# Performance work log

Hardware: AMD Instinct MI355X
Metric: run time of the kernel (lower is better)

## Reference

```python
import jax, jax.numpy as jnp
import numpy as np

NEG = -1e9  # acts as -inf in the DP while staying finite for grads


def nw_value(theta, A):
    """Soft Needleman-Wunsch terminal value with softmax (logsumexp) operator.
    theta: [N, M] match scores; A: scalar gap score.
    Recurrence: V[i,j] = theta[i-1,j-1] + logsumexp(V[i-1,j]+A, V[i-1,j-1], V[i,j-1]+A)
    with V[0,0]=0 and V[i,0]=V[0,j]=-inf.
    """
    N, M = theta.shape
    init_row = jnp.full((M + 1,), NEG, theta.dtype).at[0].set(0.0)

    def row_step(prev_row, theta_row):
        def col_step(v_left, inp):
            th, v_diag, v_up = inp
            v = th + jnp.logaddexp(jnp.logaddexp(v_up + A, v_diag), v_left + A)
            return v, v
        _, row = jax.lax.scan(
            col_step, jnp.asarray(NEG, theta.dtype),
            (theta_row, prev_row[:-1], prev_row[1:]))
        new_row = jnp.concatenate([jnp.full((1,), NEG, theta.dtype), row])
        return new_row, None

    last_row, _ = jax.lax.scan(row_step, init_row, theta)
    return last_row[M]


def nw_decode(theta, A):
    # Soft alignment matrix = dV/dtheta (expected alignment under softmax operator),
    # matching NeedlemanWunschDecoder.decode.
    return jax.grad(nw_value)(theta, A)


def setup_inputs() -> dict:
    key = jax.random.key(0)
    ks = jax.random.split(key, 7)
    B, N, M = 8, 1024, 1024
    n_alpha, n_input, n_embed = 22, 512, 512
    x = jax.random.randint(ks[0], (B, N), 0, n_alpha)
    y = jax.random.randint(ks[1], (B, M), 0, n_alpha)
    emb = jax.random.normal(ks[2], (n_alpha, n_input), jnp.float32)
    W = jax.random.normal(ks[3], (n_input, n_embed), jnp.float32) / np.sqrt(n_input)
    b = jax.random.normal(ks[4], (n_embed,), jnp.float32) * 0.01
    Wg = jax.random.normal(ks[5], (2 * n_embed, 1), jnp.float32) / np.sqrt(2 * n_embed)
    bg = jax.random.normal(ks[6], (1,), jnp.float32) * 0.01
    return {"x": x, "y": y, "emb": emb, "W": W, "b": b, "Wg": Wg, "bg": bg}


def reference(x, y, emb, W, b, Wg, bg):
    zx = emb[x] @ W + b                       # [B, N, d] embedding (EmbedLinear)
    zy = emb[y] @ W + b                       # [B, M, d]
    theta = jnp.einsum('bid,bjd->bij', zx, zy)   # [B, N, M] pairwise match scores
    merged = jnp.concatenate([zx.mean(axis=1), zy.mean(axis=1)], axis=1)  # [B, 2d]
    A = merged @ Wg + bg                      # [B, 1] gap score
    aln = jax.vmap(nw_decode)(theta, A[:, 0])    # [B, N, M]
    return jnp.swapaxes(aln, 1, 2)               # [B, M, N] (decode(...).T per batch)
```

## Files before the change

kernel.cpp:

```cpp
#include <hip/hip_runtime.h>
#include <cstdint>
#include <cstddef>

#define NEGV -1.0e9f
#define WAVES 16

__device__ __forceinline__ float lse_f(float a, float b) {
    float d = a - b;
    float m = fmaxf(a, b);
    return m + log1pf(expf(-fabsf(d)));
}
__device__ __forceinline__ float cellfwd(float th, float vu, float vdg, float vl, float A) {
    float inner = lse_f(vu + A, vdg);
    float outer = lse_f(inner, vl + A);
    return th + outer;
}

__device__ __forceinline__ void diag_geo(int d, int& st, int& L, int& tlo) {
    if (d < 64)        { st = (d * (d + 1)) >> 1;       L = d + 1;      tlo = 0; }
    else if (d < 1024) { st = 2080 + ((d - 64) << 6);   L = 64;         tlo = 0; }
    else               { int u = d - 1024;
                         st = 63520 + (u << 6) - ((u * (u + 1)) >> 1);
                         L = 63 - u;                    tlo = u + 1; }
}

__global__ void k_embed(const float* __restrict__ emb, const float* __restrict__ W,
                        const float* __restrict__ b, double* __restrict__ T) {
    int idx = blockIdx.x * blockDim.x + threadIdx.x;
    if (idx >= 22 * 512) return;
    int a = idx >> 9, d = idx & 511;
    double acc = (double)b[d];
    const float* er = emb + a * 512;
    for (int k = 0; k < 512; ++k) acc += (double)er[k] * (double)W[k * 512 + d];
    T[idx] = acc;
}

__global__ void k_gau(const double* __restrict__ T, const int* __restrict__ x,
                      const int* __restrict__ y, const float* __restrict__ Wg,
                      const float* __restrict__ bg,
                      double* __restrict__ G, double* __restrict__ Aout) {
    __shared__ double u1s[22], u2s[22];
    int t = threadIdx.x;
    if (t < 484) {
        int a = t / 22, c = t % 22;
        const double* ra = T + a * 512;
        const double* rc = T + c * 512;
        double acc = 0.0;
        for (int d = 0; d < 512; ++d) acc += ra[d] * rc[d];
        G[t] = acc;
    }
    if (t < 22) {
        double acc = 0.0;
        const double* ra = T + t * 512;
        for (int d = 0; d < 512; ++d) acc += ra[d] * (double)Wg[d];
        u1s[t] = acc;
    } else if (t >= 64 && t < 86) {
        int a = t - 64;
        double acc = 0.0;
        const double* ra = T + a * 512;
        for (int d = 0; d < 512; ++d) acc += ra[d] * (double)Wg[512 + d];
        u2s[a] = acc;
    }
    __syncthreads();
    int w = t >> 6, lane = t & 63;
    const int* xb = x + w * 1024;
    const int* yb = y + w * 1024;
    double s = 0.0;
    for (int i = lane; i < 1024; i += 64) s += u1s[xb[i]] + u2s[yb[i]];
    for (int off = 32; off > 0; off >>= 1) s += __shfl_down(s, off);
    if (lane == 0) Aout[w] = s * (1.0 / 1024.0) + (double)bg[0];
}

__global__ void k_vinit(float* __restrict__ Vbuf) {
    int b = blockIdx.x, t = threadIdx.x;
    float* Vb = Vbuf + (size_t)b * (1025 * 1025);
    Vb[t] = (t == 0) ? 0.0f : NEGV;
    if (t == 0) Vb[1024] = NEGV;
    Vb[(size_t)(t + 1) * 1025] = NEGV;
}

__global__ __launch_bounds__(1024) void k_fwdb(const int* __restrict__ x,
                                               const int* __restrict__ y,
                                               const double* __restrict__ G,
                                               const double* __restrict__ Aarr,
                                               float* __restrict__ Vbuf) {
    __shared__ float Gs[484];
    __shared__ int ys_s[1024];
    __shared__ float topbuf[WAVES][1024];
    __shared__ int prog[WAVES];

    const int b = blockIdx.x;
    const int tid = threadIdx.x;
    const int w = tid >> 6;
    const int t = tid & 63;
    float* Vb = Vbuf + (size_t)b * (1025 * 1025);

    if (tid < 484) Gs[tid] = (float)G[tid];
    ys_s[tid] = y[(b << 10) + tid];
    if (tid < WAVES) prog[tid] = 0;
    const int xs = x[(b << 10) + tid];
    __syncthreads();

    const float A = (float)Aarr[b];
    const float* Grow = Gs + xs * 22;
    float* vst = Vb + (size_t)(tid + 1) * 1025 + 1;

    float vp = NEGV;
    float vdgc = (tid == 0) ? 0.0f : NEGV;

    for (int s = 0; s < 1024 + 63; ++s) {
        if (w > 0 && s < 1024 && (s & 15) == 0) {
            const int target = (s + 16 < 1024) ? s + 16 : 1024;
            while (__hip_atomic_load(&prog[w], __ATOMIC_ACQUIRE,
                                     __HIP_MEMORY_SCOPE_WORKGROUP) < target)
                __builtin_amdgcn_s_sleep(1);
        }
        const float vu_lds = (w > 0) ? topbuf[w][(s < 1024) ? s : 1023] : NEGV;
        const float ush = __shfl_up(vp, 1);
        const int j = s - t + 1;
        if (j >= 1 && j <= 1024) {
            float vu  = (t == 0) ? vu_lds : ush;
            float v = cellfwd(Grow[ys_s[j - 1]], vu, vdgc, vp, A);
            vst[j - 1] = v;
            if (w < WAVES - 1 && t == 63) {
                topbuf[w + 1][j - 1] = v;
                if ((j & 15) == 0)
                    __hip_atomic_store(&prog[w + 1], j, __ATOMIC_RELEASE,
                                       __HIP_MEMORY_SCOPE_WORKGROUP);
            }
            vp = v; vdgc = vu;
        }
    }
}

__global__ __launch_bounds__(256) void k_wb(const double* __restrict__ Aarr,
                                            const float* __restrict__ Vbuf,
                                            float* __restrict__ bw) {
    int idx = blockIdx.x * 256 + threadIdx.x;
    int b = idx >> 20;
    int cell = idx & 1048575;
    int i = (cell >> 10) + 1;
    int j = (cell & 1023) + 1;
    const float* Vb = Vbuf + (size_t)b * (1025 * 1025);
    float vu  = Vb[(size_t)(i - 1) * 1025 + j];
    float vdg = Vb[(size_t)(i - 1) * 1025 + (j - 1)];
    float vl  = Vb[(size_t)i * 1025 + (j - 1)];
    float A = (float)Aarr[b];
    float t1 = vu + A;
    float t2 = vl + A;
    float di = t1 - vdg;
    float inner = (di > 0.f) ? (t1  + log1pf(expf(-di)))
                             : (vdg + log1pf(expf(di)));
    float dw = inner - t2;
    float outer = (dw > 0.f) ? (inner + log1pf(expf(-dw)))
                             : (t2    + log1pf(expf(dw)));
    float go1 = expf(inner - outer);
    float wlW = expf(t2 - outer);
    float wuW = go1 * expf(t1 - inner);
    float wdW = go1 * expf(vdg - inner);
    float* bbp = bw + (size_t)b * 3145728;

    if (i >= 2) {
        int rb = (i - 2) >> 4, q = (i - 2) & 15, cj = j - 1;
        int st, L, tlo; diag_geo(rb + cj, st, L, tlo);
        int f = 3 * q;
        bbp[(size_t)st * 48 + (size_t)(f >> 2) * 4 * L + ((rb - tlo) << 2) + (f & 3)] = wuW;
    }
    if (i >= 2 && j >= 2) {
        int rb = (i - 2) >> 4, q = (i - 2) & 15, cj = j - 2;
        int st, L, tlo; diag_geo(rb + cj, st, L, tlo);
        int f = 3 * q + 1;
        bbp[(size_t)st * 48 + (size_t)(f >> 2) * 4 * L + ((rb - tlo) << 2) + (f & 3)] = wdW;
    }
    if (j >= 2) {
        int rb = (i - 1) >> 4, q = (i - 1) & 15, cj = j - 2;
        int st, L, tlo; diag_geo(rb + cj, st, L, tlo);
        int f = 3 * q + 2;
        bbp[(size_t)st * 48 + (size_t)(f >> 2) * 4 * L + ((rb - tlo) << 2) + (f & 3)] = wlW;
    }
}

__global__ __launch_bounds__(64) void k_bwd16(const float* __restrict__ bw,
                                              float* __restrict__ out) {
    const int t = threadIdx.x;
    const int b = blockIdx.x;
    const float* bb = bw + (size_t)b * 3145728;
    float* ob = out + ((size_t)b << 20);
    const int r0 = t << 4;

    float e[16];
    float4 cwv[12], pfv[12];
    #pragma unroll
    for (int q = 0; q < 16; ++q) e[q] = 0.f;

    {
        int st, L, tlo; diag_geo(t + 1023, st, L, tlo);
        const float* base = bb + (size_t)st * 48;
        #pragma unroll
        for (int k = 0; k < 12; ++k)
            cwv[k] = *(const float4*)(base + (size_t)k * 4 * L);
    }

    float sdb = 0.f;
    for (int s = 0; s < 1087; ++s) {
        float dn = __shfl_down(e[0], 1);
        const int d = 1086 - s;
        const int cj = d - t;
        if (cj >= 0 && cj < 1024) {
            {
                int st, L, tlo; diag_geo(d - 1, st, L, tlo);
                const int p = t - tlo;
                const float* base = bb + (size_t)st * 48 + ((size_t)p << 2);
                #pragma unroll
                for (int k = 0; k < 12; ++k)
                    pfv[k] = *(const float4*)(base + (size_t)k * 4 * L);
            }
            const float* F = (const float*)cwv;

            float old_b = e[15];
            float eu = (t == 63) ? 0.f : dn;
            float ed = (t == 63) ? 0.f : sdb;
            float v = eu * F[45] + ed * F[46] + old_b * F[47];
            if (t == 63 && cj == 1023) v = 1.0f;
            e[15] = v;
            float new_b = v;
            #pragma unroll
            for (int q = 14; q >= 0; --q) {
                float oq = e[q];
                v = new_b * F[3 * q] + old_b * F[3 * q + 1] + oq * F[3 * q + 2];
                e[q] = v;
                new_b = v; old_b = oq;
            }
            #pragma unroll
            for (int k = 0; k < 4; ++k)
                *(float4*)&ob[(size_t)cj * 1024 + r0 + 4 * k] =
                    make_float4(e[4*k], e[4*k+1], e[4*k+2], e[4*k+3]);
            #pragma unroll
            for (int k = 0; k < 12; ++k) cwv[k] = pfv[k];
        }
        sdb = dn;
    }
}

template <bool FAITHFUL>
__global__ __launch_bounds__(1024) void k_dp(const int* __restrict__ x,
                                             const int* __restrict__ y,
                                             const double* __restrict__ G,
                                             const double* __restrict__ Aarr,
                                             float2* __restrict__ wbuf,
                                             float* __restrict__ wdbuf,
                                             float* __restrict__ out) {
    __shared__ float Gs[484];
    __shared__ int xs[1024], ys[1024];
    __shared__ float D[3][1025];
    __shared__ float E[3][1026];

    const int b = blockIdx.x;
    const int t = threadIdx.x;
    const int i = t + 1;

    if (t < 484) Gs[t] = (float)G[t];
    xs[t] = x[(b << 10) + t];
    ys[t] = y[(b << 10) + t];
    D[0][t + 1] = NEGV;
    D[1][t + 1] = NEGV;
    E[0][t] = 0.f; E[1][t] = 0.f; E[2][t] = 0.f;
    if (t == 0) {
        D[0][0] = 0.0f;
        D[1][0] = NEGV;
        E[0][1024] = 0.f; E[0][1025] = 0.f;
        E[1][1024] = 0.f; E[1][1025] = 0.f;
        E[2][1024] = 0.f; E[2][1025] = 0.f;
    }
    __syncthreads();

    const float A = (float)Aarr[b];
    const float* Grow = Gs + xs[t] * 22;
    float2* wb = wbuf + ((size_t)b << 20);
    float*  wdb = wdbuf + ((size_t)b << 20);

    for (int k = 2; k <= 2048; ++k) {
        const int cur = k % 3, p1 = (k + 2) % 3, p2 = (k + 1) % 3;
        const int j = k - i;
        if (j >= 1 && j <= 1024) {
            float vu  = D[p1][i - 1];
            float vdg = D[p2][i - 1];
            float vl  = D[p1][i];
            float t1 = vu + A;
            float t2 = vl + A;
            float di = t1 - vdg;
            float inner = (di > 0.f) ? (t1  + log1pf(expf(-di)))
                                     : (vdg + log1pf(expf(di)));
            float dw = inner - t2;
            float outer = (dw > 0.f) ? (inner + log1pf(expf(-dw)))
                                     : (t2    + log1pf(expf(dw)));
            D[cur][i] = Grow[ys[j - 1]] + outer;
            float go1 = expf(inner - outer);
            float wlW = expf(t2 - outer);
            float wuW = go1 * expf(t1 - inner);
            size_t ci = ((size_t)t << 10) + (j - 1);
            wb[ci] = make_float2(wuW, wlW);
            if (FAITHFUL) wdb[ci] = go1 * expf(vdg - inner);
        }
        if (t == 0) D[cur][0] = NEGV;
        if (i == k && k <= 1024) D[cur][k] = NEGV;
        __syncthreads();
    }

    __syncthreads();

    float* ob = out + ((size_t)b << 20);

    for (int k = 2048; k >= 2; --k) {
        const int cur = k % 3, n1 = (k + 1) % 3, n2 = (k + 2) % 3;
        const int j = k - i;
        if (j >= 1 && j <= 1024) {
            float e;
            if (k == 2048) {
                e = 1.0f;
            } else {
                float Eu = E[n1][i + 1];
                float Ed = E[n2][i + 1];
                float El = E[n1][i];
                int iw = (i < 1024) ? i : 1023;
                int jw = (j < 1024) ? j : 1023;
                float2 w_up = wb[((size_t)iw << 10) + (j - 1)];
                float2 w_lf = wb[((size_t)(i - 1) << 10) + jw];
                float w_dd;
                if (FAITHFUL) {
                    w_dd = wdb[((size_t)iw << 10) + jw];
                } else {
                    float2 w_dg = wb[((size_t)iw << 10) + jw];
                    w_dd = 1.0f - w_dg.x - w_dg.y;
                }
                e = Eu * w_up.x + Ed * w_dd + El * w_lf.y;
            }
            E[cur][i] = e;
            ob[((size_t)(j - 1) << 10) + (i - 1)] = e;
        } else {
            E[cur][i] = 0.f;
        }
        __syncthreads();
    }
}

extern "C" void kernel_launch(void* const* d_in, const int* in_sizes, int n_in,
                              void* d_out, int out_size, void* d_ws, size_t ws_size,
                              hipStream_t stream) {
    const int*   x   = (const int*)d_in[0];
    const int*   y   = (const int*)d_in[1];
    const float* emb = (const float*)d_in[2];
    const float* W   = (const float*)d_in[3];
    const float* b   = (const float*)d_in[4];
    const float* Wg  = (const float*)d_in[5];
    const float* bg  = (const float*)d_in[6];
    float* out = (float*)d_out;

    char* ws = (char*)d_ws;
    double* T    = (double*)(ws + 0);
    double* G    = (double*)(ws + 90112);
    double* Aarr = (double*)(ws + 94336);
    float*  bund = (float*)(ws + 131072);
    float2* wbuf = (float2*)(ws + 131072);
    float*  wdbuf = (float*)(ws + 131072 + ((size_t)64 << 20));
    float*  Vbuf = (float*)(ws + 131072 + ((size_t)96 << 20));

    k_embed<<<44, 256, 0, stream>>>(emb, W, b, T);
    k_gau<<<1, 512, 0, stream>>>(T, x, y, Wg, bg, G, Aarr);

    const size_t need_old = 131072 + ((size_t)96 << 20);
    const size_t need_new = need_old + (size_t)8 * 1025 * 1025 * 4;

    if (ws_size >= need_new) {
        k_vinit<<<8, 1024, 0, stream>>>(Vbuf);
        k_fwdb<<<8, 1024, 0, stream>>>(x, y, G, Aarr, Vbuf);
        k_wb<<<8 * 1024 * 1024 / 256, 256, 0, stream>>>(Aarr, Vbuf, bund);
        k_bwd16<<<8, 64, 0, stream>>>(bund, out);
    } else if (ws_size >= need_old) {
        k_dp<true><<<8, 1024, 0, stream>>>(x, y, G, Aarr, wbuf, wdbuf, out);
    } else {
        k_dp<false><<<8, 1024, 0, stream>>>(x, y, G, Aarr, wbuf, wdbuf, out);
    }
}
```

Measured before the change: 3.159 ms.

## Split forward DP across multiple workgroups per batch with global-memory flags

The forward wavefront kernel now uses four 256-thread workgroups per batch instead of one 1024-thread workgroup. Each workgroup owns 256 rows and waits on an agent-scope flag in global memory for the workgroup above. It then reads that workgroup's boundary row from the V buffer in chunks of 64 columns. This spreads the 32 blocks over more compute units and cuts per-block LDS use, at the cost of cross-workgroup spin waits, thread fences and global-memory latency on the boundary. It also risks deadlock if the dependent blocks are not co-resident.

```diff
diff --git a/kernel.cpp b/kernel.cpp
--- a/kernel.cpp
+++ b/kernel.cpp
@@ -3,7 +3,8 @@
 #include <cstddef>
 
 #define NEGV -1.0e9f
-#define WAVES 16
+#define NB 4
+#define BW 4
 
 __device__ __forceinline__ float lse_f(float a, float b) {
     float d = a - b;
@@ -71,62 +72,89 @@
     if (lane == 0) Aout[w] = s * (1.0 / 1024.0) + (double)bg[0];
 }
 
-__global__ void k_vinit(float* __restrict__ Vbuf) {
+__global__ void k_vinit(float* __restrict__ Vbuf, int* __restrict__ gflag) {
     int b = blockIdx.x, t = threadIdx.x;
     float* Vb = Vbuf + (size_t)b * (1025 * 1025);
     Vb[t] = (t == 0) ? 0.0f : NEGV;
     if (t == 0) Vb[1024] = NEGV;
     Vb[(size_t)(t + 1) * 1025] = NEGV;
-}
-
-__global__ __launch_bounds__(1024) void k_fwdb(const int* __restrict__ x,
-                                               const int* __restrict__ y,
-                                               const double* __restrict__ G,
-                                               const double* __restrict__ Aarr,
-                                               float* __restrict__ Vbuf) {
+    if (b == 0 && t < 64) gflag[t] = 0;
+}
+
+__global__ __launch_bounds__(256) void k_fwds(const int* __restrict__ x,
+                                              const int* __restrict__ y,
+                                              const double* __restrict__ G,
+                                              const double* __restrict__ Aarr,
+                                              float* __restrict__ Vbuf,
+                                              int* __restrict__ gflag) {
     __shared__ float Gs[484];
     __shared__ int ys_s[1024];
-    __shared__ float topbuf[WAVES][1024];
-    __shared__ int prog[WAVES];
-
-    const int b = blockIdx.x;
+    __shared__ float topbuf[BW][1024];
+    __shared__ int prog[BW];
+
+    const int bid = blockIdx.x;
+    const int b = bid & 7;
+    const int p = bid >> 3;
     const int tid = threadIdx.x;
     const int w = tid >> 6;
     const int t = tid & 63;
+    const int grow = (p << 8) + tid;
     float* Vb = Vbuf + (size_t)b * (1025 * 1025);
 
-    if (tid < 484) Gs[tid] = (float)G[tid];
-    ys_s[tid] = y[(b << 10) + tid];
-    if (tid < WAVES) prog[tid] = 0;
-    const int xs = x[(b << 10) + tid];
+    for (int q = tid; q < 484; q += 256) Gs[q] = (float)G[q];
+    for (int q = tid; q < 1024; q += 256) ys_s[q] = y[(b << 10) + q];
+    if (tid < BW) prog[tid] = 0;
+    const int xs = x[(b << 10) + grow];
     __syncthreads();
 
     const float A = (float)Aarr[b];
     const float* Grow = Gs + xs * 22;
-    float* vst = Vb + (size_t)(tid + 1) * 1025 + 1;
+    float* vst = Vb + (size_t)(grow + 1) * 1025 + 1;
+    const float* tsrc = Vb + (size_t)(p << 8) * 1025;
 
     float vp = NEGV;
-    float vdgc = (tid == 0) ? 0.0f : NEGV;
+    float vdgc = (p == 0 && tid == 0) ? 0.0f : NEGV;
+    float chunkv = NEGV;
+    int cbase = 0;
 
     for (int s = 0; s < 1024 + 63; ++s) {
+        if (w == 0 && p > 0 && s < 1024 && (s & 63) == 0) {
+            while (__hip_atomic_load(&gflag[(b << 2) + p - 1], __ATOMIC_ACQUIRE,
+                                     __HIP_MEMORY_SCOPE_AGENT) < s + 64)
+                __builtin_amdgcn_s_sleep(2);
+            chunkv = tsrc[s + 1 + t];
+            cbase = s;
+        }
         if (w > 0 && s < 1024 && (s & 15) == 0) {
             const int target = (s + 16 < 1024) ? s + 16 : 1024;
             while (__hip_atomic_load(&prog[w], __ATOMIC_ACQUIRE,
                                      __HIP_MEMORY_SCOPE_WORKGROUP) < target)
                 __builtin_amdgcn_s_sleep(1);
         }
-        const float vu_lds = (w > 0) ? topbuf[w][(s < 1024) ? s : 1023] : NEGV;
+        float vu_l0;
+        if (w == 0)
+            vu_l0 = (p == 0) ? NEGV : __shfl(chunkv, s - cbase);
+        else
+            vu_l0 = topbuf[w][(s < 1024) ? s : 1023];
         const float ush = __shfl_up(vp, 1);
         const int j = s - t + 1;
         if (j >= 1 && j <= 1024) {
-            float vu  = (t == 0) ? vu_lds : ush;
+            float vu = (t == 0) ? vu_l0 : ush;
             float v = cellfwd(Grow[ys_s[j - 1]], vu, vdgc, vp, A);
             vst[j - 1] = v;
-            if (w < WAVES - 1 && t == 63) {
-                topbuf[w + 1][j - 1] = v;
-                if ((j & 15) == 0)
-                    __hip_atomic_store(&prog[w + 1], j, __ATOMIC_RELEASE,
-                                       __HIP_MEMORY_SCOPE_WORKGROUP);
+            if (t == 63) {
+                if (w < BW - 1) {
+                    topbuf[w + 1][j - 1] = v;
+                    if ((j & 15) == 0)
+                        __hip_atomic_store(&prog[w + 1], j, __ATOMIC_RELEASE,
+                                           __HIP_MEMORY_SCOPE_WORKGROUP);
+                } else if (p < NB - 1) {
+                    if ((j & 63) == 0) {
+                        __threadfence();
+                        __hip_atomic_store(&gflag[(b << 2) + p], j,
+                                           __ATOMIC_RELEASE, __HIP_MEMORY_SCOPE_AGENT);
+                    }
+                }
             }
             vp = v; vdgc = vu;
         }
@@ -364,16 +392,17 @@
     float2* wbuf = (float2*)(ws + 131072);
     float*  wdbuf = (float*)(ws + 131072 + ((size_t)64 << 20));
     float*  Vbuf = (float*)(ws + 131072 + ((size_t)96 << 20));
+    int*    gflag = (int*)(ws + 131072 + ((size_t)96 << 20) + (size_t)8 * 1025 * 1025 * 4);
 
     k_embed<<<44, 256, 0, stream>>>(emb, W, b, T);
     k_gau<<<1, 512, 0, stream>>>(T, x, y, Wg, bg, G, Aarr);
 
     const size_t need_old = 131072 + ((size_t)96 << 20);
-    const size_t need_new = need_old + (size_t)8 * 1025 * 1025 * 4;
+    const size_t need_new = need_old + (size_t)8 * 1025 * 1025 * 4 + 4096;
 
     if (ws_size >= need_new) {
-        k_vinit<<<8, 1024, 0, stream>>>(Vbuf);
-        k_fwdb<<<8, 1024, 0, stream>>>(x, y, G, Aarr, Vbuf);
+        k_vinit<<<8, 1024, 0, stream>>>(Vbuf, gflag);
+        k_fwds<<<8 * NB, 256, 0, stream>>>(x, y, G, Aarr, Vbuf, gflag);
         k_wb<<<8 * 1024 * 1024 / 256, 256, 0, stream>>>(Aarr, Vbuf, bund);
         k_bwd16<<<8, 64, 0, stream>>>(bund, out);
     } else if (ws_size >= need_old) {
```

After: 2.603 ms. 1.21x faster.
